# Kernel tuning notes

Hardware: AMD Instinct MI355X
Metric: run time of the kernel (lower is better)

Reference implementation:

```python
import jax, jax.numpy as jnp
import numpy as np

D_MODEL = 1024
N_Q = 16
N_KV = 4
GRP = N_Q // N_KV
DQ = 64
DV = 64
B = 2
S = 2048
EPS = 1e-5


def _rope(x):
    # x: (N, S, ..., d) with sequence on axis 1; interleaved-pair rotary, theta=10000
    seq, d = x.shape[1], x.shape[-1]
    inv_freq = 1.0 / (10000.0 ** (jnp.arange(0, d, 2, dtype=jnp.float32) / d))
    ang = jnp.arange(seq, dtype=jnp.float32)[:, None] * inv_freq[None, :]  # (S, d/2)
    bshape = (1, seq) + (1,) * (x.ndim - 3) + (d // 2,)
    cos = jnp.cos(ang).reshape(bshape).astype(x.dtype)
    sin = jnp.sin(ang).reshape(bshape).astype(x.dtype)
    x1, x2 = x[..., 0::2], x[..., 1::2]
    r1 = x1 * cos - x2 * sin
    r2 = x1 * sin + x2 * cos
    return jnp.stack([r1, r2], axis=-1).reshape(x.shape)


def _layer_norm(x, gamma, beta):
    mu = jnp.mean(x, axis=-1, keepdims=True)
    var = jnp.var(x, axis=-1, keepdims=True)
    return (x - mu) * jax.lax.rsqrt(var + EPS) * gamma + beta


def setup_inputs() -> dict:
    key = jax.random.key(0)
    ks = jax.random.split(key, 13)
    scale = 0.02
    return {
        "query_sequences": jax.random.normal(ks[0], (B, S, D_MODEL), jnp.float32),
        "key_sequences": jax.random.normal(ks[1], (B, S, D_MODEL), jnp.float32),
        "value_sequences": jax.random.normal(ks[2], (B, S, D_MODEL), jnp.float32),
        "key_value_sequence_lengths": jax.random.randint(ks[3], (B,), S // 2, S + 1),
        "ln_gamma": jnp.ones((D_MODEL,), jnp.float32),
        "ln_beta": jnp.zeros((D_MODEL,), jnp.float32),
        "Wq": jax.random.normal(ks[4], (D_MODEL, N_Q * DQ), jnp.float32) * scale,
        "bq": jnp.zeros((N_Q * DQ,), jnp.float32),
        "Wk": jax.random.normal(ks[5], (D_MODEL, N_KV * DQ), jnp.float32) * scale,
        "bk": jnp.zeros((N_KV * DQ,), jnp.float32),
        "Wv": jax.random.normal(ks[6], (D_MODEL, N_KV * DV), jnp.float32) * scale,
        "bv": jnp.zeros((N_KV * DV,), jnp.float32),
        "Wo": jax.random.normal(ks[7], (N_Q * DV, D_MODEL), jnp.float32) * scale,
        "bo": jnp.zeros((D_MODEL,), jnp.float32),
    }


def reference(query_sequences, key_sequences, value_sequences,
              key_value_sequence_lengths, ln_gamma, ln_beta,
              Wq, bq, Wk, bk, Wv, bv, Wo, bo):
    N, t = query_sequences.shape[0], query_sequences.shape[1]
    T = key_sequences.shape[1]
    # pre-LN (self-attn: applied to q, k, v inputs)
    q_in = _layer_norm(query_sequences, ln_gamma, ln_beta)
    k_in = _layer_norm(key_sequences, ln_gamma, ln_beta)
    v_in = _layer_norm(value_sequences, ln_gamma, ln_beta)
    q = (q_in @ Wq + bq).reshape(N, t, N_KV, GRP, DQ)      # (N,t,h,H,d)
    k = (k_in @ Wk + bk).reshape(N, T, N_KV, DQ)           # (N,T,h,d)
    v = (v_in @ Wv + bv).reshape(N, T, N_KV, DV)           # (N,T,h,d)
    q = _rope(q)
    k = _rope(k)
    scores = jnp.einsum('nthHd,nThd->nhHtT', q, k) / jnp.sqrt(jnp.float32(DQ))
    key_pos = jnp.arange(T)
    pad_ok = (key_pos[None, :] < key_value_sequence_lengths[:, None])  # (N,T)
    causal_ok = (jnp.arange(t)[:, None] >= key_pos[None, :])           # (t,T)
    mask = pad_ok[:, None, None, None, :] & causal_ok[None, None, None, :, :]
    scores = jnp.where(mask, scores, -jnp.inf)
    attn = jax.nn.softmax(scores, axis=-1)                 # (N,h,H,t,T)
    attn_viz = jnp.transpose(attn, (0, 2, 1, 3, 4))        # (N,H,h,t,T)
    seq = jnp.einsum('nhHtT,nThd->nthHd', attn, v).reshape(N, t, N_Q * DV)
    out = seq @ Wo + bo
    return out, attn_viz
```

## Files before the change

kernel.cpp:

```cpp
#include <hip/hip_runtime.h>
#include <hip/hip_bf16.h>

#define S_LEN 2048
#define DM 1024

typedef __attribute__((ext_vector_type(8))) short s16x8;
typedef __attribute__((ext_vector_type(4))) float f32x4;
typedef __attribute__((ext_vector_type(4))) ushort u16x4;

__device__ __forceinline__ ushort f2bf(float f){
  union { float f; unsigned u; } v; v.f = f;
  unsigned r = (v.u + 0x7FFFu + ((v.u >> 16) & 1u)) >> 16;
  return (ushort)r;
}

__device__ __forceinline__ f32x4 mfma16(s16x8 a, s16x8 b, f32x4 c){
  return __builtin_amdgcn_mfma_f32_16x16x32_bf16(a, b, c, 0, 0, 0);
}

__device__ __forceinline__ void gl_lds16(const ushort* g, ushort* l){
  __builtin_amdgcn_global_load_lds(
      (const __attribute__((address_space(1))) unsigned int*)g,
      (__attribute__((address_space(3))) unsigned int*)l, 16, 0, 0);
}

__global__ __launch_bounds__(256) void trig_kernel(float* __restrict__ tab){
  int idx = blockIdx.x*256 + threadIdx.x;
  int t = idx >> 5, i2 = idx & 31;
  float inv = exp2f(-(float)i2 * 0.4152410118609203f);
  float ang = (float)t * inv;
  tab[2*idx]   = cosf(ang);
  tab[2*idx+1] = sinf(ang);
}

__global__ __launch_bounds__(256) void ln3_kernel(const float* __restrict__ x0,
    const float* __restrict__ x1, const float* __restrict__ x2,
    const float* __restrict__ g, const float* __restrict__ be, ushort* __restrict__ o){
  int row = blockIdx.x;
  int tid = threadIdx.x;
  const float* xs = (blockIdx.y==0) ? x0 : (blockIdx.y==1) ? x1 : x2;
  const float* xr = xs + (size_t)row*DM;
  float4 xv = *(const float4*)(xr + tid*4);
  float s  = xv.x+xv.y+xv.z+xv.w;
  float s2 = xv.x*xv.x+xv.y*xv.y+xv.z*xv.z+xv.w*xv.w;
  for (int m=1;m<64;m<<=1){ s += __shfl_xor(s,m); s2 += __shfl_xor(s2,m); }
  __shared__ float red[8];
  int w = tid>>6, l = tid&63;
  if (l==0){ red[w]=s; red[4+w]=s2; }
  __syncthreads();
  float ts = red[0]+red[1]+red[2]+red[3];
  float t2 = red[4]+red[5]+red[6]+red[7];
  float mu  = ts*(1.0f/DM);
  float var = t2*(1.0f/DM) - mu*mu;
  float rs  = rsqrtf(var + 1e-5f);
  float vals[4] = {xv.x,xv.y,xv.z,xv.w};
  const float* gp = g + tid*4;
  const float* bp = be + tid*4;
  u16x4 ov;
  #pragma unroll
  for (int j=0;j<4;j++) ov[j] = f2bf((vals[j]-mu)*rs*gp[j] + bp[j]);
  *(u16x4*)(o + (size_t)blockIdx.y*4194304 + (size_t)row*DM + tid*4) = ov;
}

__global__ __launch_bounds__(256) void wtr_kernel(const float* __restrict__ in,
    ushort* __restrict__ out, int N){
  __shared__ float lsf[32][36];
  int tid = threadIdx.x;
  int n0 = blockIdx.x*32, k0 = blockIdx.y*32;
  int kr = tid>>3, nc = (tid&7)*4;
  float4 v = *(const float4*)(in + (size_t)(k0+kr)*N + n0 + nc);
  *(float4*)&lsf[kr][nc] = v;
  __syncthreads();
  int nr = tid>>3, kc = (tid&7)*4;
  u16x4 o;
  #pragma unroll
  for (int j=0;j<4;j++) o[j] = f2bf(lsf[kc+j][nr]);
  *(u16x4*)(out + (size_t)(n0+nr)*DM + k0 + kc) = o;
}

__global__ __launch_bounds__(256) void utr_kernel(const ushort* __restrict__ kvb,
    ushort* __restrict__ vt){
  __shared__ ushort lst[64*72];
  int tid = threadIdx.x;
  int t0 = blockIdx.x*64;
  int y = blockIdx.y; int n = y>>2, h = y&3;
  int Tr = tid>>2, dg = (tid&3)*16;
  const ushort* ip = kvb + ((size_t)(n*S_LEN + t0 + Tr))*512 + 256 + h*64 + dg;
  *(s16x8*)&lst[Tr*72 + dg]     = *(const s16x8*)ip;
  *(s16x8*)&lst[Tr*72 + dg + 8] = *(const s16x8*)(ip+8);
  __syncthreads();
  int d = tid>>2, Tg = (tid&3)*16;
  ushort* op = vt + ((size_t)(y*64 + d))*S_LEN + t0 + Tg;
  #pragma unroll
  for (int q=0;q<4;q++){
    u16x4 o;
    #pragma unroll
    for (int j=0;j<4;j++) o[j] = lst[(Tg+4*q+j)*72 + d];
    *(u16x4*)(op + 4*q) = o;
  }
}

template<int BM, int MODE>
__global__ __launch_bounds__(256) void gemm_kernel(
    const ushort* __restrict__ A, const ushort* __restrict__ A2,
    const ushort* __restrict__ BT, const float* __restrict__ bias,
    const float* __restrict__ bias2, const float* __restrict__ tab,
    void* __restrict__ Cv, int N, int K){
  constexpr int MF = 2;
  constexpr int NF = (BM == 128) ? 4 : 2;
  constexpr int ACALLS = BM/32;
  __shared__ ushort Als[BM*64];
  __shared__ ushort Bls[64*64];
  int tid = threadIdx.x;
  int w = tid>>6, l = tid&63, lg = l>>4, li = l&15;
  int wrow = (BM==128) ? w*32 : (w>>1)*32;
  int wcol = (BM==128) ? 0 : (w&1)*32;
  int mbase = blockIdx.y*BM, nbase = blockIdx.x*64;
  const ushort* Ause = A;
  if (MODE==2 && nbase >= 256) Ause = A2;
  f32x4 acc[MF][NF];
  #pragma unroll
  for (int m=0;m<MF;m++)
    #pragma unroll
    for (int n=0;n<NF;n++) acc[m][n] = (f32x4){0.f,0.f,0.f,0.f};
  for (int kk=0; kk<K; kk+=64){
    __syncthreads();
    #pragma unroll
    for (int s=0;s<ACALLS;s++){
      int idx = s*256 + tid;
      int row = idx>>3, ch = idx&7;
      gl_lds16(Ause + (size_t)(mbase+row)*K + kk + 8*(ch ^ (row&7)),
               &Als[(size_t)(s*256 + w*64)*8]);
    }
    #pragma unroll
    for (int s=0;s<2;s++){
      int idx = s*256 + tid;
      int row = idx>>3, ch = idx&7;
      gl_lds16(BT + (size_t)(nbase+row)*K + kk + 8*(ch ^ (row&7)),
               &Bls[(size_t)(s*256 + w*64)*8]);
    }
    __syncthreads();
    #pragma unroll
    for (int f=0;f<2;f++){
      s16x8 af[MF], bfv[NF];
      #pragma unroll
      for (int m=0;m<MF;m++)
        af[m] = *(const s16x8*)&Als[(wrow+m*16+li)*64 + 8*((lg+4*f) ^ (li&7))];
      #pragma unroll
      for (int n=0;n<NF;n++)
        bfv[n] = *(const s16x8*)&Bls[(wcol+n*16+li)*64 + 8*((lg+4*f) ^ (li&7))];
      #pragma unroll
      for (int m=0;m<MF;m++)
        #pragma unroll
        for (int n=0;n<NF;n++)
          acc[m][n] = mfma16(af[m], bfv[n], acc[m][n]);
    }
  }
  bool doRope = (MODE==1) || (MODE==2 && nbase < 256);
  #pragma unroll
  for (int n=0;n<NF;n++){
    int gcol = nbase + wcol + n*16 + li;
    float bv0 = (MODE==2 && nbase>=256) ? bias2[gcol-256] : bias[gcol];
    #pragma unroll
    for (int m=0;m<MF;m++){
      #pragma unroll
      for (int r=0;r<4;r++){
        int grow = mbase + wrow + m*16 + 4*lg + r;
        float val = acc[m][n][r] + bv0;
        if (doRope){
          int t = grow & (S_LEN-1);
          int d = gcol & 63;
          const float* tp = tab + t*64 + (d & 62);
          float cv = tp[0], sv = tp[1];
          float other = __shfl_xor(val, 1);
          val = (d & 1) ? (other*sv + val*cv) : (val*cv - other*sv);
        }
        if (MODE==3) ((float*)Cv)[(size_t)grow*N + gcol] = val;
        else         ((ushort*)Cv)[(size_t)grow*N + gcol] = f2bf(val);
      }
    }
  }
}

__global__ __launch_bounds__(256) void flash_kernel(
    const ushort* __restrict__ qg, const ushort* __restrict__ kvb,
    const ushort* __restrict__ vt, const int* __restrict__ lens,
    ushort* __restrict__ seq, float* __restrict__ mbuf, float* __restrict__ lbuf){
  __shared__ ushort kls[128*72];
  __shared__ ushort vls[64*136];
  __shared__ ushort pls[64*136];
  int tid = threadIdx.x;
  int w = tid>>6, l = tid&63, lg = l>>4, li = l&15;
  int qbase = blockIdx.x*64;
  int qh = blockIdx.y;
  int n  = blockIdx.z;
  int h = qh>>2;
  int len = lens[n];
  const float L2E = 1.4426950408889634f;

  int trow = qbase + 16*w + li;
  const ushort* qp = qg + ((size_t)n*S_LEN + trow)*1024 + qh*64 + 8*lg;
  s16x8 qf0 = *(const s16x8*)qp;
  s16x8 qf1 = *(const s16x8*)(qp + 32);

  int sT2 = tid>>1, sd2 = (tid&1)*32;
  int dv  = tid>>2, tc  = (tid&3)*32;
  const ushort* kp = kvb + ((size_t)n*S_LEN + sT2)*512 + h*64 + sd2;
  const ushort* vp = vt + ((size_t)((n*4+h)*64 + dv))*S_LEN + tc;

  float m_r[4], l_r[4];
  f32x4 oacc[4];
  #pragma unroll
  for (int r=0;r<4;r++){ m_r[r] = -1e30f; l_r[r] = 0.f; }
  #pragma unroll
  for (int c=0;c<4;c++) oacc[c] = (f32x4){0.f,0.f,0.f,0.f};
  int Tlim = min(qbase + 63, len - 1);
  int nR = (Tlim >> 7) + 1;

  for (int it=0; it<nR; ++it){
    int Tb = it*128;
    __syncthreads();
    { const ushort* kpp = kp + (size_t)Tb*512;
      #pragma unroll
      for (int j=0;j<4;j++)
        *(s16x8*)&kls[sT2*72 + sd2 + 8*j] = *(const s16x8*)(kpp + 8*j);
      const ushort* vpp = vp + Tb;
      #pragma unroll
      for (int j=0;j<4;j++)
        *(s16x8*)&vls[dv*136 + tc + 8*j] = *(const s16x8*)(vpp + 8*j);
    }
    __syncthreads();
    f32x4 sc[8];
    #pragma unroll
    for (int c=0;c<8;c++) sc[c] = (f32x4){0.f,0.f,0.f,0.f};
    __builtin_amdgcn_s_setprio(1);
    #pragma unroll
    for (int c=0;c<8;c++){
      s16x8 b0 = *(const s16x8*)&kls[(16*c+li)*72 + 8*lg];
      s16x8 b1 = *(const s16x8*)&kls[(16*c+li)*72 + 8*lg + 32];
      sc[c] = mfma16(qf0, b0, sc[c]);
      sc[c] = mfma16(qf1, b1, sc[c]);
    }
    __builtin_amdgcn_s_setprio(0);
    #pragma unroll
    for (int c=0;c<8;c++){
      int Tg = Tb + 16*c + li;
      bool colp = Tg < len;
      #pragma unroll
      for (int r=0;r<4;r++){
        int tg = qbase + 16*w + 4*lg + r;
        sc[c][r] = (colp && Tg <= tg) ? sc[c][r]*0.125f : -1e30f;
      }
    }
    float sf[4];
    #pragma unroll
    for (int r=0;r<4;r++){
      float tmax = sc[0][r];
      #pragma unroll
      for (int c=1;c<8;c++) tmax = fmaxf(tmax, sc[c][r]);
      for (int msk=1; msk<16; msk<<=1) tmax = fmaxf(tmax, __shfl_xor(tmax, msk));
      float mn = fmaxf(m_r[r], tmax);
      float ssum = 0.f;
      #pragma unroll
      for (int c=0;c<8;c++){ sc[c][r] = exp2f((sc[c][r]-mn)*L2E); ssum += sc[c][r]; }
      for (int msk=1; msk<16; msk<<=1) ssum += __shfl_xor(ssum, msk);
      sf[r] = exp2f((m_r[r]-mn)*L2E);
      l_r[r] = l_r[r]*sf[r] + ssum;
      m_r[r] = mn;
    }
    #pragma unroll
    for (int c=0;c<4;c++)
      #pragma unroll
      for (int r=0;r<4;r++) oacc[c][r] *= sf[r];
    #pragma unroll
    for (int c=0;c<8;c++)
      #pragma unroll
      for (int r=0;r<4;r++)
        pls[(16*w + 4*lg + r)*136 + 16*c + li] = f2bf(sc[c][r]);
    __builtin_amdgcn_s_setprio(1);
    #pragma unroll
    for (int f=0; f<4; f++){
      s16x8 pa = *(const s16x8*)&pls[(16*w + li)*136 + 8*lg + 32*f];
      #pragma unroll
      for (int c=0;c<4;c++){
        s16x8 vf = *(const s16x8*)&vls[(16*c+li)*136 + 8*lg + 32*f];
        oacc[c] = mfma16(pa, vf, oacc[c]);
      }
    }
    __builtin_amdgcn_s_setprio(0);
  }

  float inv_l[4];
  #pragma unroll
  for (int r=0;r<4;r++) inv_l[r] = 1.0f / l_r[r];
  #pragma unroll
  for (int c=0;c<4;c++){
    #pragma unroll
    for (int r=0;r<4;r++){
      int tg = qbase + 16*w + 4*lg + r;
      seq[((size_t)n*S_LEN + tg)*1024 + qh*64 + 16*c + li] = f2bf(oacc[c][r]*inv_l[r]);
    }
  }
  int zi = n*16 + qh;
  if (li == 0){
    #pragma unroll
    for (int r=0;r<4;r++){
      int tg = qbase + 16*w + 4*lg + r;
      mbuf[(size_t)zi*S_LEN + tg] = m_r[r];
      lbuf[(size_t)zi*S_LEN + tg] = inv_l[r];
    }
  }
}

__global__ __launch_bounds__(256) void viz_kernel(
    const ushort* __restrict__ qg, const ushort* __restrict__ kvb,
    const int* __restrict__ lens, const float* __restrict__ mbuf,
    const float* __restrict__ lbuf, float* __restrict__ viz){
  __shared__ ushort kls[64*72];
  int tid = threadIdx.x;
  int Tb0 = blockIdx.x*256;
  int qbase = blockIdx.y*64;
  int zi = blockIdx.z;
  int n = zi>>4, qh = zi&15;
  int h = qh>>2, H = qh&3;
  int len = lens[n];
  float* vizp = viz + (size_t)((n*4 + H)*4 + h) * S_LEN * S_LEN;
  int w = tid>>6, l = tid&63, lg = l>>4, li = l&15;
  const float L2E = 1.4426950408889634f;

  bool anyComp = (Tb0 <= qbase + 63) && (Tb0 < len);
  s16x8 qf0, qf1;
  float m_r[4], il_r[4];
  if (anyComp){
    int trow = qbase + 16*w + li;
    const ushort* qp = qg + ((size_t)n*S_LEN + trow)*1024 + qh*64 + 8*lg;
    qf0 = *(const s16x8*)qp;
    qf1 = *(const s16x8*)(qp + 32);
    #pragma unroll
    for (int r=0;r<4;r++){
      int tg = qbase + 16*w + 4*lg + r;
      m_r[r]  = mbuf[(size_t)zi*S_LEN + tg];
      il_r[r] = lbuf[(size_t)zi*S_LEN + tg];
    }
  }

  int sT = tid>>2, sdg = (tid&3)*16;
  for (int s=0; s<4; ++s){
    int Tb = Tb0 + s*64;
    bool zero = (Tb > qbase + 63) || (Tb >= len);
    if (zero){
      int row = qbase + (tid>>2);
      float* zp = vizp + (size_t)row*S_LEN + Tb + (tid&3)*16;
      f32x4 zv = (f32x4){0.f,0.f,0.f,0.f};
      #pragma unroll
      for (int u=0;u<4;u++) *(f32x4*)(zp + 4*u) = zv;
      continue;
    }
    __syncthreads();
    { const ushort* kpp = kvb + ((size_t)n*S_LEN + Tb + sT)*512 + h*64 + sdg;
      *(s16x8*)&kls[sT*72 + sdg]     = *(const s16x8*)kpp;
      *(s16x8*)&kls[sT*72 + sdg + 8] = *(const s16x8*)(kpp + 8);
    }
    __syncthreads();
    f32x4 sc[4];
    #pragma unroll
    for (int c=0;c<4;c++) sc[c] = (f32x4){0.f,0.f,0.f,0.f};
    #pragma unroll
    for (int c=0;c<4;c++){
      s16x8 b0 = *(const s16x8*)&kls[(16*c+li)*72 + 8*lg];
      s16x8 b1 = *(const s16x8*)&kls[(16*c+li)*72 + 8*lg + 32];
      sc[c] = mfma16(qf0, b0, sc[c]);
      sc[c] = mfma16(qf1, b1, sc[c]);
    }
    #pragma unroll
    for (int c=0;c<4;c++){
      int Tg = Tb + 16*c + li;
      bool colp = Tg < len;
      #pragma unroll
      for (int r=0;r<4;r++){
        int tg = qbase + 16*w + 4*lg + r;
        bool ok = colp && (Tg <= tg);
        float p = ok ? exp2f((sc[c][r]*0.125f - m_r[r])*L2E) * il_r[r] : 0.f;
        vizp[(size_t)tg*S_LEN + Tg] = p;
      }
    }
  }
}

extern "C" void kernel_launch(void* const* d_in, const int* in_sizes, int n_in,
                              void* d_out, int out_size, void* d_ws, size_t ws_size,
                              hipStream_t stream){
  const float* xq = (const float*)d_in[0];
  const float* xk = (const float*)d_in[1];
  const float* xv = (const float*)d_in[2];
  const int*  lens= (const int*)d_in[3];
  const float* g  = (const float*)d_in[4];
  const float* be = (const float*)d_in[5];
  const float* Wq = (const float*)d_in[6];
  const float* bq = (const float*)d_in[7];
  const float* Wk = (const float*)d_in[8];
  const float* bk = (const float*)d_in[9];
  const float* Wv = (const float*)d_in[10];
  const float* bv = (const float*)d_in[11];
  const float* Wo = (const float*)d_in[12];
  const float* bo = (const float*)d_in[13];

  ushort* ws  = (ushort*)d_ws;
  ushort* xnq = ws;
  ushort* xnk = ws + 4194304;
  ushort* xnv = ws + 8388608;
  ushort* qb  = ws + 12582912;
  ushort* kvb = ws + 16777216;
  ushort* vt  = ws + 18874368;
  ushort* WqT = ws + 19922944;
  ushort* WkvT= ws + 20971520;
  ushort* WoT = ws + 21495808;
  float*  tab = (float*)(ws + 22544384);
  float*  mbuf= (float*)(ws + 22806528);
  float*  lbuf= (float*)(ws + 22937600);
  ushort* seqb = xnq;

  float* outp = (float*)d_out;
  float* vizp = outp + (size_t)4194304;

  trig_kernel<<<256,256,0,stream>>>(tab);
  ln3_kernel<<<dim3(4096,3),256,0,stream>>>(xq, xk, xv, g, be, xnq);
  wtr_kernel<<<dim3(32,32),256,0,stream>>>(Wq, WqT, 1024);
  wtr_kernel<<<dim3( 8,32),256,0,stream>>>(Wk, WkvT, 256);
  wtr_kernel<<<dim3( 8,32),256,0,stream>>>(Wv, WkvT + (size_t)256*1024, 256);
  wtr_kernel<<<dim3(32,32),256,0,stream>>>(Wo, WoT, 1024);
  gemm_kernel<128,1><<<dim3(16,32),256,0,stream>>>(xnq, nullptr, WqT, bq, nullptr, tab, qb, 1024, 1024);
  gemm_kernel< 64,2><<<dim3( 8,64),256,0,stream>>>(xnk, xnv, WkvT, bk, bv, tab, kvb, 512, 1024);
  utr_kernel<<<dim3(32,8),256,0,stream>>>(kvb, vt);
  flash_kernel<<<dim3(32,16,2),256,0,stream>>>(qb, kvb, vt, lens, seqb, mbuf, lbuf);
  viz_kernel<<<dim3(8,32,32),256,0,stream>>>(qb, kvb, lens, mbuf, lbuf, vizp);
  gemm_kernel<128,3><<<dim3(16,32),256,0,stream>>>(seqb, nullptr, WoT, bo, nullptr, tab, (void*)outp, 1024, 1024);
}
```

Before: 847.5 us.

## Fuse attention-probability output into flash kernel and merge weight transposes

Result: slower. 1.024 ms (+20.8%).

```diff
diff --git a/kernel.cpp b/kernel.cpp
--- a/kernel.cpp
+++ b/kernel.cpp
@@ -62,11 +62,23 @@
   *(u16x4*)(o + (size_t)blockIdx.y*4194304 + (size_t)row*DM + tid*4) = ov;
 }
 
-__global__ __launch_bounds__(256) void wtr_kernel(const float* __restrict__ in,
-    ushort* __restrict__ out, int N){
+__global__ __launch_bounds__(256) void wtr4_kernel(
+    const float* __restrict__ Wq, const float* __restrict__ Wo,
+    const float* __restrict__ Wk, const float* __restrict__ Wv,
+    ushort* __restrict__ WqT, ushort* __restrict__ WoT, ushort* __restrict__ WkvT){
+  int z = blockIdx.z;
+  int bx = blockIdx.x;
+  const float* in; ushort* out; int N;
+  if (z==0){ in=Wq; out=WqT; N=1024; }
+  else if (z==1){ in=Wo; out=WoT; N=1024; }
+  else {
+    if (bx < 8){ in=Wk; out=WkvT; N=256; }
+    else if (bx < 16){ in=Wv; out=WkvT + (size_t)256*1024; N=256; bx-=8; }
+    else return;
+  }
   __shared__ float lsf[32][36];
   int tid = threadIdx.x;
-  int n0 = blockIdx.x*32, k0 = blockIdx.y*32;
+  int n0 = bx*32, k0 = blockIdx.y*32;
   int kr = tid>>3, nc = (tid&7)*4;
   float4 v = *(const float4*)(in + (size_t)(k0+kr)*N + n0 + nc);
   *(float4*)&lsf[kr][nc] = v;
@@ -182,10 +194,10 @@
   }
 }
 
-__global__ __launch_bounds__(256) void flash_kernel(
+__global__ __launch_bounds__(256) void attn_kernel(
     const ushort* __restrict__ qg, const ushort* __restrict__ kvb,
     const ushort* __restrict__ vt, const int* __restrict__ lens,
-    ushort* __restrict__ seq, float* __restrict__ mbuf, float* __restrict__ lbuf){
+    ushort* __restrict__ seq, float* __restrict__ viz){
   __shared__ ushort kls[128*72];
   __shared__ ushort vls[64*136];
   __shared__ ushort pls[64*136];
@@ -194,9 +206,10 @@
   int qbase = blockIdx.x*64;
   int qh = blockIdx.y;
   int n  = blockIdx.z;
-  int h = qh>>2;
+  int h = qh>>2, H = qh&3;
   int len = lens[n];
   const float L2E = 1.4426950408889634f;
+  float* vizp = viz + (size_t)((n*4 + H)*4 + h) * S_LEN * S_LEN;
 
   int trow = qbase + 16*w + li;
   const ushort* qp = qg + ((size_t)n*S_LEN + trow)*1024 + qh*64 + 8*lg;
@@ -217,19 +230,25 @@
   int Tlim = min(qbase + 63, len - 1);
   int nR = (Tlim >> 7) + 1;
 
+  s16x8 kreg[4], vreg[4];
+  #pragma unroll
+  for (int j=0;j<4;j++){ kreg[j] = *(const s16x8*)(kp + 8*j); vreg[j] = *(const s16x8*)(vp + 8*j); }
+
   for (int it=0; it<nR; ++it){
+    __syncthreads();
+    #pragma unroll
+    for (int j=0;j<4;j++){
+      *(s16x8*)&kls[sT2*72 + sd2 + 8*j] = kreg[j];
+      *(s16x8*)&vls[dv*136 + tc + 8*j]  = vreg[j];
+    }
+    if (it+1 < nR){
+      const ushort* kpp = kp + (size_t)(it+1)*128*512;
+      const ushort* vpp = vp + (it+1)*128;
+      #pragma unroll
+      for (int j=0;j<4;j++){ kreg[j] = *(const s16x8*)(kpp + 8*j); vreg[j] = *(const s16x8*)(vpp + 8*j); }
+    }
+    __syncthreads();
     int Tb = it*128;
-    __syncthreads();
-    { const ushort* kpp = kp + (size_t)Tb*512;
-      #pragma unroll
-      for (int j=0;j<4;j++)
-        *(s16x8*)&kls[sT2*72 + sd2 + 8*j] = *(const s16x8*)(kpp + 8*j);
-      const ushort* vpp = vp + Tb;
-      #pragma unroll
-      for (int j=0;j<4;j++)
-        *(s16x8*)&vls[dv*136 + tc + 8*j] = *(const s16x8*)(vpp + 8*j);
-    }
-    __syncthreads();
     f32x4 sc[8];
     #pragma unroll
     for (int c=0;c<8;c++) sc[c] = (f32x4){0.f,0.f,0.f,0.f};
@@ -301,89 +320,55 @@
       seq[((size_t)n*S_LEN + tg)*1024 + qh*64 + 16*c + li] = f2bf(oacc[c][r]*inv_l[r]);
     }
   }
-  int zi = n*16 + qh;
-  if (li == 0){
-    #pragma unroll
-    for (int r=0;r<4;r++){
-      int tg = qbase + 16*w + 4*lg + r;
-      mbuf[(size_t)zi*S_LEN + tg] = m_r[r];
-      lbuf[(size_t)zi*S_LEN + tg] = inv_l[r];
-    }
-  }
-}
-
-__global__ __launch_bounds__(256) void viz_kernel(
-    const ushort* __restrict__ qg, const ushort* __restrict__ kvb,
-    const int* __restrict__ lens, const float* __restrict__ mbuf,
-    const float* __restrict__ lbuf, float* __restrict__ viz){
-  __shared__ ushort kls[64*72];
-  int tid = threadIdx.x;
-  int Tb0 = blockIdx.x*256;
-  int qbase = blockIdx.y*64;
-  int zi = blockIdx.z;
-  int n = zi>>4, qh = zi&15;
-  int h = qh>>2, H = qh&3;
-  int len = lens[n];
-  float* vizp = viz + (size_t)((n*4 + H)*4 + h) * S_LEN * S_LEN;
-  int w = tid>>6, l = tid&63, lg = l>>4, li = l&15;
-  const float L2E = 1.4426950408889634f;
-
-  bool anyComp = (Tb0 <= qbase + 63) && (Tb0 < len);
-  s16x8 qf0, qf1;
-  float m_r[4], il_r[4];
-  if (anyComp){
-    int trow = qbase + 16*w + li;
-    const ushort* qp = qg + ((size_t)n*S_LEN + trow)*1024 + qh*64 + 8*lg;
-    qf0 = *(const s16x8*)qp;
-    qf1 = *(const s16x8*)(qp + 32);
-    #pragma unroll
-    for (int r=0;r<4;r++){
-      int tg = qbase + 16*w + 4*lg + r;
-      m_r[r]  = mbuf[(size_t)zi*S_LEN + tg];
-      il_r[r] = lbuf[(size_t)zi*S_LEN + tg];
-    }
-  }
-
-  int sT = tid>>2, sdg = (tid&3)*16;
-  for (int s=0; s<4; ++s){
-    int Tb = Tb0 + s*64;
-    bool zero = (Tb > qbase + 63) || (Tb >= len);
-    if (zero){
-      int row = qbase + (tid>>2);
-      float* zp = vizp + (size_t)row*S_LEN + Tb + (tid&3)*16;
-      f32x4 zv = (f32x4){0.f,0.f,0.f,0.f};
-      #pragma unroll
-      for (int u=0;u<4;u++) *(f32x4*)(zp + 4*u) = zv;
-      continue;
-    }
-    __syncthreads();
-    { const ushort* kpp = kvb + ((size_t)n*S_LEN + Tb + sT)*512 + h*64 + sdg;
-      *(s16x8*)&kls[sT*72 + sdg]     = *(const s16x8*)kpp;
-      *(s16x8*)&kls[sT*72 + sdg + 8] = *(const s16x8*)(kpp + 8);
-    }
-    __syncthreads();
-    f32x4 sc[4];
-    #pragma unroll
-    for (int c=0;c<4;c++) sc[c] = (f32x4){0.f,0.f,0.f,0.f};
-    #pragma unroll
-    for (int c=0;c<4;c++){
+
+  #pragma unroll
+  for (int j=0;j<4;j++) kreg[j] = *(const s16x8*)(kp + 8*j);
+  for (int it=0; it<nR; ++it){
+    __syncthreads();
+    #pragma unroll
+    for (int j=0;j<4;j++)
+      *(s16x8*)&kls[sT2*72 + sd2 + 8*j] = kreg[j];
+    if (it+1 < nR){
+      const ushort* kpp = kp + (size_t)(it+1)*128*512;
+      #pragma unroll
+      for (int j=0;j<4;j++) kreg[j] = *(const s16x8*)(kpp + 8*j);
+    }
+    __syncthreads();
+    int Tb = it*128;
+    f32x4 sc[8];
+    #pragma unroll
+    for (int c=0;c<8;c++) sc[c] = (f32x4){0.f,0.f,0.f,0.f};
+    __builtin_amdgcn_s_setprio(1);
+    #pragma unroll
+    for (int c=0;c<8;c++){
       s16x8 b0 = *(const s16x8*)&kls[(16*c+li)*72 + 8*lg];
       s16x8 b1 = *(const s16x8*)&kls[(16*c+li)*72 + 8*lg + 32];
       sc[c] = mfma16(qf0, b0, sc[c]);
       sc[c] = mfma16(qf1, b1, sc[c]);
     }
-    #pragma unroll
-    for (int c=0;c<4;c++){
+    __builtin_amdgcn_s_setprio(0);
+    #pragma unroll
+    for (int c=0;c<8;c++){
       int Tg = Tb + 16*c + li;
       bool colp = Tg < len;
       #pragma unroll
       for (int r=0;r<4;r++){
         int tg = qbase + 16*w + 4*lg + r;
         bool ok = colp && (Tg <= tg);
-        float p = ok ? exp2f((sc[c][r]*0.125f - m_r[r])*L2E) * il_r[r] : 0.f;
-        vizp[(size_t)tg*S_LEN + Tg] = p;
+        float p = ok ? exp2f((sc[c][r]*0.125f - m_r[r])*L2E) * inv_l[r] : 0.f;
+        __builtin_nontemporal_store(p, &vizp[(size_t)tg*S_LEN + Tg]);
       }
     }
+  }
+
+  int zrow = qbase + (tid>>2);
+  int zc = (tid&3)*16;
+  f32x4 zv = (f32x4){0.f,0.f,0.f,0.f};
+  for (int T0 = nR*128; T0 < S_LEN; T0 += 64){
+    float* zp = vizp + (size_t)zrow*S_LEN + T0 + zc;
+    #pragma unroll
+    for (int u=0;u<4;u++)
+      __builtin_nontemporal_store(zv, (f32x4*)(zp + 4*u));
   }
 }
 
@@ -416,8 +401,6 @@
   ushort* WkvT= ws + 20971520;
   ushort* WoT = ws + 21495808;
   float*  tab = (float*)(ws + 22544384);
-  float*  mbuf= (float*)(ws + 22806528);
-  float*  lbuf= (float*)(ws + 22937600);
   ushort* seqb = xnq;
 
   float* outp = (float*)d_out;
@@ -425,14 +408,10 @@
 
   trig_kernel<<<256,256,0,stream>>>(tab);
   ln3_kernel<<<dim3(4096,3),256,0,stream>>>(xq, xk, xv, g, be, xnq);
-  wtr_kernel<<<dim3(32,32),256,0,stream>>>(Wq, WqT, 1024);
-  wtr_kernel<<<dim3( 8,32),256,0,stream>>>(Wk, WkvT, 256);
-  wtr_kernel<<<dim3( 8,32),256,0,stream>>>(Wv, WkvT + (size_t)256*1024, 256);
-  wtr_kernel<<<dim3(32,32),256,0,stream>>>(Wo, WoT, 1024);
+  wtr4_kernel<<<dim3(32,32,3),256,0,stream>>>(Wq, Wo, Wk, Wv, WqT, WoT, WkvT);
   gemm_kernel<128,1><<<dim3(16,32),256,0,stream>>>(xnq, nullptr, WqT, bq, nullptr, tab, qb, 1024, 1024);
   gemm_kernel< 64,2><<<dim3( 8,64),256,0,stream>>>(xnk, xnv, WkvT, bk, bv, tab, kvb, 512, 1024);
   utr_kernel<<<dim3(32,8),256,0,stream>>>(kvb, vt);
-  flash_kernel<<<dim3(32,16,2),256,0,stream>>>(qb, kvb, vt, lens, seqb, mbuf, lbuf);
-  viz_kernel<<<dim3(8,32,32),256,0,stream>>>(qb, kvb, lens, mbuf, lbuf, vizp);
+  attn_kernel<<<dim3(32,16,2),256,0,stream>>>(qb, kvb, vt, lens, seqb, vizp);
   gemm_kernel<128,3><<<dim3(16,32),256,0,stream>>>(seqb, nullptr, WoT, bo, nullptr, tab, (void*)outp, 1024, 1024);
 }
```
